# Kernel optimization log

Measured on AMD Instinct MI355X. Metric: run time of the kernel, lower is better.

The kernel has to match this reference:

```python
import jax, jax.numpy as jnp
import numpy as np

LAM = 1e-05
NUM_POINTS = 300
THRESHOLD = 0.5


def _sobel(img):
    # img: [B, 1, H, W] -> edge magnitude [B, 1, H, W]
    kx = jnp.array([[-1., 0., 1.], [-2., 0., 2.], [-1., 0., 1.]], jnp.float32).reshape(1, 1, 3, 3)
    ky = jnp.array([[-1., -2., -1.], [0., 0., 0.], [1., 2., 1.]], jnp.float32).reshape(1, 1, 3, 3)
    dn = jax.lax.conv_dimension_numbers(img.shape, kx.shape, ('NCHW', 'OIHW', 'NCHW'))
    ex = jax.lax.conv_general_dilated(img, kx, (1, 1), ((1, 1), (1, 1)), dimension_numbers=dn)
    ey = jax.lax.conv_general_dilated(img, ky, (1, 1), ((1, 1), (1, 1)), dimension_numbers=dn)
    return jnp.sqrt(ex ** 2 + ey ** 2)


def _select_points(edge_map, key):
    # JIT-friendly analogue of nonzero + randperm[:300]: random scores on
    # above-threshold pixels, take top NUM_POINTS; invalid slots are padded
    # with a duplicate of the first valid point (zero-length MST edges, so
    # they contribute nothing to total persistence, matching fewer points).
    H, W = edge_map.shape
    flat = edge_map.reshape(-1)
    mask = flat > THRESHOLD
    scores = jnp.where(mask, jax.random.uniform(key, flat.shape), -jnp.inf)
    _, idx = jax.lax.top_k(scores, NUM_POINTS)
    valid = mask[idx]
    pts = jnp.stack([idx // W, idx % W], axis=-1).astype(jnp.float32)  # (row, col)
    pts = jnp.where(valid[:, None], pts, pts[0])
    return pts


def _mst_total_persistence(pts):
    # H0 persistence of a Vietoris-Rips complex: births are 0, deaths are the
    # MST edge lengths (Prim's algorithm via lax.scan over N-1 steps).
    # total_persistence with exponent q=2: sum(death^2).
    d2 = jnp.sum((pts[:, None, :] - pts[None, :, :]) ** 2, axis=-1)
    D = jnp.sqrt(jnp.maximum(d2, 0.0))  # [N, N]
    n = pts.shape[0]
    in_tree = jnp.zeros((n,), dtype=bool).at[0].set(True)

    def step(carry, _):
        in_tree, mind = carry
        m = jnp.where(in_tree, jnp.inf, mind)
        j = jnp.argmin(m)
        w = m[j]
        in_tree = in_tree.at[j].set(True)
        mind = jnp.minimum(mind, D[j])
        return (in_tree, mind), w

    _, deaths = jax.lax.scan(step, (in_tree, D[0]), None, length=n - 1)
    return jnp.sum(deaths ** 2)


def _topo_loss(model_output, labels):
    pred_edges = _sobel(jax.nn.sigmoid(model_output))[:, 0]  # [B, H, W]
    mask_edges = _sobel(labels)[:, 0]                         # [B, H, W]
    B = pred_edges.shape[0]
    keys = jax.random.split(jax.random.key(42), 2 * B).reshape(B, 2)

    def per_sample(pe, me, k):
        pts_p = _select_points(pe, k[0])
        pts_m = _select_points(me, k[1])
        tp_p = _mst_total_persistence(pts_p)
        tp_m = _mst_total_persistence(pts_m)
        # SummaryStatisticLoss(total_persistence): |stat(mask) - stat(pred)|
        return jnp.abs(tp_m - tp_p)

    losses = jax.vmap(per_sample)(pred_edges, mask_edges, keys)
    return LAM * jnp.sum(losses) / B


def setup_inputs() -> dict:
    key = jax.random.key(0)
    k1, k2 = jax.random.split(key)
    model_output = jax.random.normal(k1, (32, 1, 512, 512), dtype=jnp.float32)
    labels = jax.random.uniform(k2, (32, 1, 512, 512), dtype=jnp.float32)
    return {"model_output": model_output, "labels": labels}


def reference(model_output, labels):
    return _topo_loss(model_output, labels)
```

## Files before the change

### kernel.cpp

```cpp
#include <hip/hip_runtime.h>
#include <cstdint>
#include <cstddef>

#define NPIX (512 * 512)
#define NMAPS 64
#define NPTS 300
#define CAP 2048
#define LCAP 640
#define NWORDS 4096
#define TARGET 700.0
#define MT_FIXED 8340608u

__device__ __forceinline__ uint32_t umin32(uint32_t a, uint32_t b) {
  return a < b ? a : b;
}

__device__ __forceinline__ void tf2x32(uint32_t k0, uint32_t k1,
                                       uint32_t x0, uint32_t x1,
                                       uint32_t& o0, uint32_t& o1) {
  uint32_t ks2 = k0 ^ k1 ^ 0x1BD11BDAu;
#define TFR(r) { x0 += x1; x1 = (x1 << (r)) | (x1 >> (32 - (r))); x1 ^= x0; }
  x0 += k0; x1 += k1;
  TFR(13) TFR(15) TFR(26) TFR(6)
  x0 += k1; x1 += ks2 + 1u;
  TFR(17) TFR(29) TFR(16) TFR(24)
  x0 += ks2; x1 += k0 + 2u;
  TFR(13) TFR(15) TFR(26) TFR(6)
  x0 += k0; x1 += k1 + 3u;
  TFR(17) TFR(29) TFR(16) TFR(24)
  x0 += k1; x1 += ks2 + 4u;
  TFR(13) TFR(15) TFR(26) TFR(6)
  x0 += ks2; x1 += k0 + 5u;
#undef TFR
  o0 = x0; o1 = x1;
}

__device__ __forceinline__ uint32_t score23(uint32_t k0, uint32_t k1, uint32_t p) {
  uint32_t a, b;
  tf2x32(k0, k1, 0u, p, a, b);
  return (a ^ b) >> 9;
}

__device__ __forceinline__ void map_key(int m, uint32_t& k0, uint32_t& k1) {
  tf2x32(0u, 42u, 0u, (uint32_t)m, k0, k1);
}

template <int CTRL>
__device__ __forceinline__ uint32_t dpp_mov_u32(uint32_t x) {
  return (uint32_t)__builtin_amdgcn_update_dpp((int)x, (int)x, CTRL, 0xF, 0xF,
                                               false);
}

__device__ __forceinline__ uint32_t wave_min_u32_bcast(uint32_t v) {
  v = umin32(v, dpp_mov_u32<0x111>(v));
  v = umin32(v, dpp_mov_u32<0x112>(v));
  v = umin32(v, dpp_mov_u32<0x114>(v));
  v = umin32(v, dpp_mov_u32<0x118>(v));
  v = umin32(v, dpp_mov_u32<0x142>(v));
  v = umin32(v, dpp_mov_u32<0x143>(v));
  return (uint32_t)__builtin_amdgcn_readlane((int)v, 63);
}

__global__ __launch_bounds__(256) void edge_collect_kernel(
    const float* __restrict__ mo, const float* __restrict__ lb,
    unsigned long long* __restrict__ bitmap, unsigned int* __restrict__ wcnts,
    unsigned long long* __restrict__ cand, unsigned int* __restrict__ gcnt32) {
  const int m = blockIdx.y;
  const int which = m & 1;
  const float* __restrict__ src = (which ? lb : mo) + (size_t)(m >> 1) * NPIX;
  const int l = threadIdx.x & 63;
  const int wi = blockIdx.x * 4 + (threadIdx.x >> 6);
  const int cs = wi & 7;
  const int seg = wi >> 3;
  const int y0 = seg * 32;
  const int X = cs * 64 + l;
  const int hcol = (l == 0) ? X - 1 : ((l == 63) ? X + 1 : -1);

  __shared__ unsigned long long lbuf[LCAP];
  __shared__ unsigned int lcnt;
  __shared__ unsigned int lbase;
  if (threadIdx.x == 0) lcnt = 0;
  __syncthreads();

  uint32_t k0, k1;
  map_key(m, k0, k1);

  auto sig = [&](float t) { return which ? t : 1.f / (1.f + expf(-t)); };
  auto ldmain = [&](int row) -> float {
    return ((unsigned)row < 512u) ? sig(src[row * 512 + X]) : 0.f;
  };
  auto ldhalo = [&](int row) -> float {
    return ((unsigned)row < 512u && (unsigned)hcol < 512u)
               ? sig(src[row * 512 + hcol]) : 0.f;
  };

  float a = ldmain(y0 - 1), ha = ldhalo(y0 - 1);
  float b = ldmain(y0),     hb = ldhalo(y0);
  unsigned int cnt = 0;

  for (int i = 0; i < 32; ++i) {
    const int y = y0 + i;
    float c = ldmain(y + 1), hc = ldhalo(y + 1);

    float aL = __shfl_up(a, 1);   if (l == 0)  aL = ha;
    float aR = __shfl_down(a, 1); if (l == 63) aR = ha;
    float bL = __shfl_up(b, 1);   if (l == 0)  bL = hb;
    float bR = __shfl_down(b, 1); if (l == 63) bR = hb;
    float cL = __shfl_up(c, 1);   if (l == 0)  cL = hc;
    float cR = __shfl_down(c, 1); if (l == 63) cR = hc;

    float ex = (aR - aL) + 2.f * (bR - bL) + (cR - cL);
    float ey = (cL + 2.f * c + cR) - (aL + 2.f * a + aR);
    float edge = sqrtf(ex * ex + ey * ey);
    bool bit = edge > 0.5f;

    unsigned long long ball = __ballot(bit);
    if (l == 0) {
      bitmap[(size_t)m * NWORDS + (size_t)y * 8 + cs] = ball;
      cnt += (unsigned int)__popcll(ball);
    }
    if (bit) {
      uint32_t p = (uint32_t)(y * 512 + X);
      uint32_t sc = score23(k0, k1, p);
      if (sc >= MT_FIXED) {
        unsigned int pos = atomicAdd(&lcnt, 1u);
        if (pos < LCAP)
          lbuf[pos] = ((unsigned long long)sc << 32) | (uint32_t)(~p);
      }
    }
    a = b; ha = hb; b = c; hb = hc;
  }
  if (l == 0) wcnts[m * 128 + wi] = cnt;

  __syncthreads();
  unsigned int cc = lcnt < LCAP ? lcnt : LCAP;
  if (threadIdx.x == 0)
    lbase = atomicAdd(&gcnt32[m * 32], lcnt + (lcnt > LCAP ? 0x1000000u : 0u));
  __syncthreads();
  for (unsigned int i = threadIdx.x; i < cc; i += 256) {
    unsigned int pos = lbase + i;
    if (pos < CAP) cand[(size_t)m * CAP + pos] = lbuf[i];
  }
}

__device__ __forceinline__ void reduce_N(const unsigned int* __restrict__ wcnts,
                                         int m, int tid, unsigned int* sN) {
  if (tid < 64) {
    unsigned int v = wcnts[m * 128 + tid] + wcnts[m * 128 + 64 + tid];
#pragma unroll
    for (int off = 32; off > 0; off >>= 1) v += __shfl_xor(v, off, 64);
    if (tid == 0) *sN = v;
  }
}

__global__ __launch_bounds__(256) void select_kernel(
    const unsigned long long* __restrict__ bitmap,
    const unsigned int* __restrict__ wcnts,
    const unsigned long long* __restrict__ cand,
    const unsigned int* __restrict__ gcnt32,
    uint32_t* __restrict__ pts, unsigned int* __restrict__ nsel) {
  const int m = blockIdx.x;
  const int tid = threadIdx.x;
  __shared__ unsigned long long buf[CAP];
  __shared__ unsigned int hist[256];
  __shared__ unsigned int s_tot, s_cnt, s_b, s_rank, sN;

  reduce_N(wcnts, m, tid, &sN);
  __syncthreads();
  const unsigned int N = sN;
  if (N == 0) { if (tid == 0) nsel[m] = 0; return; }
  const unsigned int need = N < NPTS ? N : NPTS;

  unsigned int c;
  const unsigned int g = gcnt32[m * 32];
  if (g >= need && g <= CAP) {
    c = g;
    for (unsigned int i = tid; i < c; i += 256)
      buf[i] = cand[(size_t)m * CAP + i];
    __syncthreads();
  } else {
    uint32_t k0, k1;
    map_key(m, k0, k1);
    const unsigned long long* __restrict__ wmap = bitmap + (size_t)m * NWORDS;
    unsigned int mt = 0, cnt = 0;
    double target = TARGET;
    for (int iter = 0; iter < 16; ++iter) {
      mt = ((double)N > target)
               ? (unsigned int)(8388608.0 * (1.0 - target / (double)N))
               : 0u;
      if (tid == 0) s_tot = 0;
      __syncthreads();
      unsigned int lc = 0;
      for (int w = tid; w < NWORDS; w += 256) {
        unsigned long long word = wmap[w];
        while (word) {
          int bpos = __builtin_ctzll(word);
          word &= word - 1;
          uint32_t p = ((uint32_t)w << 6) + (uint32_t)bpos;
          lc += (score23(k0, k1, p) >= mt) ? 1u : 0u;
        }
      }
      if (lc) atomicAdd(&s_tot, lc);
      __syncthreads();
      cnt = s_tot;
      __syncthreads();
      if (cnt >= need && cnt <= CAP) break;
      if (cnt < need) target *= 3.0; else target *= 0.5;
    }
    if (tid == 0) s_cnt = 0;
    __syncthreads();
    for (int w = tid; w < NWORDS; w += 256) {
      unsigned long long word = wmap[w];
      while (word) {
        int bpos = __builtin_ctzll(word);
        word &= word - 1;
        uint32_t p = ((uint32_t)w << 6) + (uint32_t)bpos;
        uint32_t sc = score23(k0, k1, p);
        if (sc >= mt) {
          unsigned int pos = atomicAdd(&s_cnt, 1u);
          if (pos < CAP)
            buf[pos] = ((unsigned long long)sc << 32) | (uint32_t)(~p);
        }
      }
    }
    __syncthreads();
    c = s_cnt < CAP ? s_cnt : CAP;
    __syncthreads();
  }

  unsigned long long T = 0ull;
  if (c > need) {
    unsigned int rank = need;
    unsigned long long prefix = 0ull;
    for (int sh = 48; sh >= 0; sh -= 8) {
      hist[tid] = 0;
      __syncthreads();
      for (unsigned int i = tid; i < c; i += 256) {
        unsigned long long k = buf[i];
        if ((k >> (sh + 8)) == (prefix >> (sh + 8)))
          atomicAdd(&hist[(unsigned int)(k >> sh) & 255u], 1u);
      }
      __syncthreads();
      if (tid < 64) {
        unsigned int h0 = hist[4 * tid], h1 = hist[4 * tid + 1];
        unsigned int h2 = hist[4 * tid + 2], h3 = hist[4 * tid + 3];
        unsigned int gsum = h0 + h1 + h2 + h3;
        unsigned int s = gsum;
#pragma unroll
        for (int off = 1; off < 64; off <<= 1) {
          unsigned int o = __shfl_down(s, off, 64);
          s += (tid + off < 64) ? o : 0u;
        }
        unsigned int above = s - gsum;
        unsigned int S3 = above, S2 = S3 + h3, S1 = S2 + h2, S0 = S1 + h1;
        if (S3 < rank && rank <= S3 + h3) { s_b = 4 * tid + 3; s_rank = rank - S3; }
        if (S2 < rank && rank <= S2 + h2) { s_b = 4 * tid + 2; s_rank = rank - S2; }
        if (S1 < rank && rank <= S1 + h1) { s_b = 4 * tid + 1; s_rank = rank - S1; }
        if (S0 < rank && rank <= S0 + h0) { s_b = 4 * tid + 0; s_rank = rank - S0; }
      }
      __syncthreads();
      prefix |= ((unsigned long long)s_b) << sh;
      rank = s_rank;
    }
    T = prefix;
  }

  if (tid == 0) s_cnt = 0;
  __syncthreads();
  for (unsigned int i = tid; i < c; i += 256) {
    unsigned long long k = buf[i];
    if (k >= T) {
      unsigned int pos = atomicAdd(&s_cnt, 1u);
      if (pos < NPTS) {
        uint32_t p = ~(uint32_t)k;
        pts[(size_t)m * NPTS + pos] = ((p >> 9) << 16) | (p & 511u);
      }
    }
  }
  __syncthreads();
  if (tid == 0) nsel[m] = s_cnt < need ? s_cnt : need;
}

__global__ __launch_bounds__(64, 1) void mst_kernel(
    const uint32_t* __restrict__ pts, const unsigned int* __restrict__ nsel,
    float* __restrict__ tps) {
  const int m = blockIdx.x;
  const int l = threadIdx.x;
  const int n = (int)nsel[m];
  if (n <= 1) { if (l == 0) tps[m] = 0.f; return; }

  uint32_t pk[5], key[5];
  int px[5], py[5];
#pragma unroll
  for (int k = 0; k < 5; ++k) {
    int id = k * 64 + l;
    pk[k] = (id < n) ? pts[(size_t)m * NPTS + id] : 0u;
  }
  const uint32_t p0 = (uint32_t)__builtin_amdgcn_readlane((int)pk[0], 0);
  const int x0 = (int)(p0 >> 16), y0 = (int)(p0 & 0xFFFFu);
#pragma unroll
  for (int k = 0; k < 5; ++k) {
    int id = k * 64 + l;
    px[k] = (int)(pk[k] >> 16);
    py[k] = (int)(pk[k] & 0xFFFFu);
    if (id > 0 && id < n) {
      int dx = px[k] - x0, dy = py[k] - y0;
      key[k] = ((uint32_t)(__mul24(dx, dx) + __mul24(dy, dy)) << 9) |
               (uint32_t)id;
    } else {
      key[k] = 0xFFFFFFFFu;
    }
  }

  float tp = 0.f;
  for (int it = 0; it < n - 1; ++it) {
    uint32_t best = umin32(umin32(umin32(key[0], key[1]),
                                  umin32(key[2], key[3])), key[4]);
    best = wave_min_u32_bcast(best);
    tp += (float)(best >> 9);
    const int j = (int)(best & 511u);
    const int ko = j >> 6, lo = j & 63;
    uint32_t cp = pk[0];
#pragma unroll
    for (int k = 1; k < 5; ++k) cp = (ko == k) ? pk[k] : cp;
    const uint32_t pj = (uint32_t)__builtin_amdgcn_readlane((int)cp, lo);
    const int jx = (int)(pj >> 16), jy = (int)(pj & 0xFFFFu);
#pragma unroll
    for (int k = 0; k < 5; ++k) {
      int dx = px[k] - jx, dy = py[k] - jy;
      uint32_t nk = ((uint32_t)(__mul24(dx, dx) + __mul24(dy, dy)) << 9) |
                    (uint32_t)(k * 64 + l);
      uint32_t upd = (key[k] == 0xFFFFFFFFu) ? 0xFFFFFFFFu : umin32(key[k], nk);
      key[k] = (k == ko && l == lo) ? 0xFFFFFFFFu : upd;
    }
  }
  if (l == 0) tps[m] = tp;
}

__global__ void finalize_kernel(const float* __restrict__ tps,
                                float* __restrict__ out) {
  const int tid = threadIdx.x;
  float v = 0.f;
  if (tid < 32) v = fabsf(tps[2 * tid + 1] - tps[2 * tid]);
#pragma unroll
  for (int off = 32; off > 0; off >>= 1) v += __shfl_xor(v, off, 64);
  if (tid == 0) out[0] = 1e-5f * v / 32.f;
}

extern "C" void kernel_launch(void* const* d_in, const int* in_sizes, int n_in,
                              void* d_out, int out_size, void* d_ws,
                              size_t ws_size, hipStream_t stream) {
  const float* mo = (const float*)d_in[0];
  const float* lb = (const float*)d_in[1];
  float* out = (float*)d_out;
  char* ws = (char*)d_ws;

  unsigned long long* bitmap = (unsigned long long*)ws;
  unsigned long long* cand = (unsigned long long*)(ws + 2097152);
  unsigned int* wcnts  = (unsigned int*)(ws + 3145728);
  unsigned int* gcnt32 = (unsigned int*)(ws + 3178496);
  unsigned int* nsel   = (unsigned int*)(ws + 3186688);
  float* tps           = (float*)(ws + 3186944);
  uint32_t* pts        = (uint32_t*)(ws + 3187200);

  hipMemsetAsync(gcnt32, 0, 8192, stream);
  edge_collect_kernel<<<dim3(32, 64), 256, 0, stream>>>(mo, lb, bitmap, wcnts,
                                                        cand, gcnt32);
  select_kernel<<<NMAPS, 256, 0, stream>>>(bitmap, wcnts, cand, gcnt32, pts,
                                           nsel);
  mst_kernel<<<NMAPS, 64, 0, stream>>>(pts, nsel, tps);
  finalize_kernel<<<1, 64, 0, stream>>>(tps, out);
}
```

Before: 253.9 us.

## Fuse finalize into MST kernel, tighten candidate threshold, use fast sigmoid

Removes the separate finalize kernel. Each MST block now handles a pred/mask pair in two waves and atomically adds its scaled loss term into the output, which the edge kernel zeroes first. Several smaller changes come with it: the candidate score threshold is raised and the candidate capacity halved, the sigmoid uses __expf, the MST sum is kept as an integer, and the sqrt in the edge test becomes a squared comparison. A tighter candidate threshold risks falling back to a slower path, or missing points, when fewer candidates pass. The float atomic accumulation makes the summation order nondeterministic.

```diff
diff --git a/kernel.cpp b/kernel.cpp
--- a/kernel.cpp
+++ b/kernel.cpp
@@ -5,11 +5,11 @@
 #define NPIX (512 * 512)
 #define NMAPS 64
 #define NPTS 300
-#define CAP 2048
+#define CAP 1024
 #define LCAP 640
 #define NWORDS 4096
 #define TARGET 700.0
-#define MT_FIXED 8340608u
+#define MT_FIXED 8368608u
 
 __device__ __forceinline__ uint32_t umin32(uint32_t a, uint32_t b) {
   return a < b ? a : b;
@@ -64,7 +64,8 @@
 __global__ __launch_bounds__(256) void edge_collect_kernel(
     const float* __restrict__ mo, const float* __restrict__ lb,
     unsigned long long* __restrict__ bitmap, unsigned int* __restrict__ wcnts,
-    unsigned long long* __restrict__ cand, unsigned int* __restrict__ gcnt32) {
+    unsigned long long* __restrict__ cand, unsigned int* __restrict__ gcnt32,
+    float* __restrict__ out) {
   const int m = blockIdx.y;
   const int which = m & 1;
   const float* __restrict__ src = (which ? lb : mo) + (size_t)(m >> 1) * NPIX;
@@ -76,6 +77,8 @@
   const int X = cs * 64 + l;
   const int hcol = (l == 0) ? X - 1 : ((l == 63) ? X + 1 : -1);
 
+  if (m == 0 && blockIdx.x == 0 && threadIdx.x == 0) out[0] = 0.f;
+
   __shared__ unsigned long long lbuf[LCAP];
   __shared__ unsigned int lcnt;
   __shared__ unsigned int lbase;
@@ -85,7 +88,9 @@
   uint32_t k0, k1;
   map_key(m, k0, k1);
 
-  auto sig = [&](float t) { return which ? t : 1.f / (1.f + expf(-t)); };
+  auto sig = [&](float t) {
+    return which ? t : 1.f / (1.f + __expf(-t));
+  };
   auto ldmain = [&](int row) -> float {
     return ((unsigned)row < 512u) ? sig(src[row * 512 + X]) : 0.f;
   };
@@ -111,8 +116,7 @@
 
     float ex = (aR - aL) + 2.f * (bR - bL) + (cR - cL);
     float ey = (cL + 2.f * c + cR) - (aL + 2.f * a + aR);
-    float edge = sqrtf(ex * ex + ey * ey);
-    bool bit = edge > 0.5f;
+    bool bit = (ex * ex + ey * ey) > 0.25f;
 
     unsigned long long ball = __ballot(bit);
     if (l == 0) {
@@ -281,70 +285,67 @@
   if (tid == 0) nsel[m] = s_cnt < need ? s_cnt : need;
 }
 
-__global__ __launch_bounds__(64, 1) void mst_kernel(
+__global__ __launch_bounds__(128, 1) void mst_kernel(
     const uint32_t* __restrict__ pts, const unsigned int* __restrict__ nsel,
-    float* __restrict__ tps) {
-  const int m = blockIdx.x;
-  const int l = threadIdx.x;
+    float* __restrict__ out) {
+  const int wv = threadIdx.x >> 6;
+  const int m = blockIdx.x * 2 + wv;
+  const int l = threadIdx.x & 63;
   const int n = (int)nsel[m];
-  if (n <= 1) { if (l == 0) tps[m] = 0.f; return; }
-
-  uint32_t pk[5], key[5];
-  int px[5], py[5];
-#pragma unroll
-  for (int k = 0; k < 5; ++k) {
-    int id = k * 64 + l;
-    pk[k] = (id < n) ? pts[(size_t)m * NPTS + id] : 0u;
-  }
-  const uint32_t p0 = (uint32_t)__builtin_amdgcn_readlane((int)pk[0], 0);
-  const int x0 = (int)(p0 >> 16), y0 = (int)(p0 & 0xFFFFu);
-#pragma unroll
-  for (int k = 0; k < 5; ++k) {
-    int id = k * 64 + l;
-    px[k] = (int)(pk[k] >> 16);
-    py[k] = (int)(pk[k] & 0xFFFFu);
-    if (id > 0 && id < n) {
-      int dx = px[k] - x0, dy = py[k] - y0;
-      key[k] = ((uint32_t)(__mul24(dx, dx) + __mul24(dy, dy)) << 9) |
-               (uint32_t)id;
-    } else {
-      key[k] = 0xFFFFFFFFu;
-    }
-  }
-
-  float tp = 0.f;
-  for (int it = 0; it < n - 1; ++it) {
-    uint32_t best = umin32(umin32(umin32(key[0], key[1]),
-                                  umin32(key[2], key[3])), key[4]);
-    best = wave_min_u32_bcast(best);
-    tp += (float)(best >> 9);
-    const int j = (int)(best & 511u);
-    const int ko = j >> 6, lo = j & 63;
-    uint32_t cp = pk[0];
-#pragma unroll
-    for (int k = 1; k < 5; ++k) cp = (ko == k) ? pk[k] : cp;
-    const uint32_t pj = (uint32_t)__builtin_amdgcn_readlane((int)cp, lo);
-    const int jx = (int)(pj >> 16), jy = (int)(pj & 0xFFFFu);
+  __shared__ float stp[2];
+
+  unsigned int utp = 0;
+  if (n > 1) {
+    uint32_t pk[5], key[5];
+    int px[5], py[5];
 #pragma unroll
     for (int k = 0; k < 5; ++k) {
-      int dx = px[k] - jx, dy = py[k] - jy;
-      uint32_t nk = ((uint32_t)(__mul24(dx, dx) + __mul24(dy, dy)) << 9) |
-                    (uint32_t)(k * 64 + l);
-      uint32_t upd = (key[k] == 0xFFFFFFFFu) ? 0xFFFFFFFFu : umin32(key[k], nk);
-      key[k] = (k == ko && l == lo) ? 0xFFFFFFFFu : upd;
-    }
-  }
-  if (l == 0) tps[m] = tp;
-}
-
-__global__ void finalize_kernel(const float* __restrict__ tps,
-                                float* __restrict__ out) {
-  const int tid = threadIdx.x;
-  float v = 0.f;
-  if (tid < 32) v = fabsf(tps[2 * tid + 1] - tps[2 * tid]);
-#pragma unroll
-  for (int off = 32; off > 0; off >>= 1) v += __shfl_xor(v, off, 64);
-  if (tid == 0) out[0] = 1e-5f * v / 32.f;
+      int id = k * 64 + l;
+      pk[k] = (id < n) ? pts[(size_t)m * NPTS + id] : 0u;
+    }
+    const uint32_t p0 = (uint32_t)__builtin_amdgcn_readlane((int)pk[0], 0);
+    const int x0 = (int)(p0 >> 16), y0 = (int)(p0 & 0xFFFFu);
+#pragma unroll
+    for (int k = 0; k < 5; ++k) {
+      int id = k * 64 + l;
+      px[k] = (int)(pk[k] >> 16);
+      py[k] = (int)(pk[k] & 0xFFFFu);
+      if (id > 0 && id < n) {
+        int dx = px[k] - x0, dy = py[k] - y0;
+        key[k] = ((uint32_t)(__mul24(dx, dx) + __mul24(dy, dy)) << 9) |
+                 (uint32_t)id;
+      } else {
+        key[k] = 0xFFFFFFFFu;
+      }
+    }
+
+    for (int it = 0; it < n - 1; ++it) {
+      uint32_t best = umin32(umin32(umin32(key[0], key[1]),
+                                    umin32(key[2], key[3])), key[4]);
+      best = wave_min_u32_bcast(best);
+      utp += best >> 9;
+      const int j = (int)(best & 511u);
+      const int ko = j >> 6, lo = j & 63;
+      uint32_t cp = pk[0];
+#pragma unroll
+      for (int k = 1; k < 5; ++k) cp = (ko == k) ? pk[k] : cp;
+      const uint32_t pj = (uint32_t)__builtin_amdgcn_readlane((int)cp, lo);
+      const int jx = (int)(pj >> 16), jy = (int)(pj & 0xFFFFu);
+#pragma unroll
+      for (int k = 0; k < 5; ++k) {
+        int dx = px[k] - jx, dy = py[k] - jy;
+        uint32_t nk = ((uint32_t)(__mul24(dx, dx) + __mul24(dy, dy)) << 9) |
+                      (uint32_t)(k * 64 + l);
+        uint32_t upd =
+            (key[k] == 0xFFFFFFFFu) ? 0xFFFFFFFFu : umin32(key[k], nk);
+        key[k] = (k == ko && l == lo) ? 0xFFFFFFFFu : upd;
+      }
+    }
+  }
+  if (l == 0) stp[wv] = (float)utp;
+  __syncthreads();
+  if (threadIdx.x == 0)
+    atomicAdd(out, 1e-5f * fabsf(stp[1] - stp[0]) / 32.f);
 }
 
 extern "C" void kernel_launch(void* const* d_in, const int* in_sizes, int n_in,
@@ -357,17 +358,15 @@
 
   unsigned long long* bitmap = (unsigned long long*)ws;
   unsigned long long* cand = (unsigned long long*)(ws + 2097152);
-  unsigned int* wcnts  = (unsigned int*)(ws + 3145728);
-  unsigned int* gcnt32 = (unsigned int*)(ws + 3178496);
-  unsigned int* nsel   = (unsigned int*)(ws + 3186688);
-  float* tps           = (float*)(ws + 3186944);
-  uint32_t* pts        = (uint32_t*)(ws + 3187200);
+  unsigned int* wcnts  = (unsigned int*)(ws + 2621440);
+  unsigned int* gcnt32 = (unsigned int*)(ws + 2654208);
+  unsigned int* nsel   = (unsigned int*)(ws + 2662400);
+  uint32_t* pts        = (uint32_t*)(ws + 2662656);
 
   hipMemsetAsync(gcnt32, 0, 8192, stream);
   edge_collect_kernel<<<dim3(32, 64), 256, 0, stream>>>(mo, lb, bitmap, wcnts,
-                                                        cand, gcnt32);
+                                                        cand, gcnt32, out);
   select_kernel<<<NMAPS, 256, 0, stream>>>(bitmap, wcnts, cand, gcnt32, pts,
                                            nsel);
-  mst_kernel<<<NMAPS, 64, 0, stream>>>(pts, nsel, tps);
-  finalize_kernel<<<1, 64, 0, stream>>>(tps, out);
-}
+  mst_kernel<<<32, 128, 0, stream>>>(pts, nsel, out);
+}
```

After: 246.8 us. -2.8%, faster.
